# Kernel tuning notes

Hardware: AMD Instinct MI355X
Metric: run time of the kernel (lower is better)

## Reference

```python
import jax, jax.numpy as jnp
import numpy as np

B, H, W, C, NH, WS, SS = 16, 112, 112, 384, 12, 7, 3
HD = C // NH          # head dim = 32
N = WS * WS           # tokens per window = 49
MLP_H = 4 * C         # 1536
NW = (H // WS) * (W // WS)  # windows per image = 256


def _rel_pos_index():
    coords = np.stack(np.meshgrid(np.arange(WS), np.arange(WS), indexing='ij')).reshape(2, -1)
    rel = (coords[:, :, None] - coords[:, None, :]).transpose(1, 2, 0)  # (N, N, 2)
    rel[..., 0] += WS - 1
    rel[..., 1] += WS - 1
    rel[..., 0] *= 2 * WS - 1
    return rel.sum(-1)  # (N, N) in [0, (2WS-1)^2)


def _attn_mask():
    img = np.zeros((H, W))
    cnt = 0
    slices = (slice(0, -WS), slice(-WS, -SS), slice(-SS, None))
    for hs in slices:
        for ws_ in slices:
            img[hs, ws_] = cnt
            cnt += 1
    mw = img.reshape(H // WS, WS, W // WS, WS).transpose(0, 2, 1, 3).reshape(-1, N)
    am = mw[:, None, :] - mw[:, :, None]
    return np.where(am != 0, -100.0, 0.0).astype(np.float32)  # (NW, N, N)


REL_IDX = jnp.asarray(_rel_pos_index().reshape(-1))  # (N*N,) int
MASK = jnp.asarray(_attn_mask())                      # (NW, N, N)


def _ln(x, g, b, eps=1e-5):
    m = jnp.mean(x, -1, keepdims=True)
    v = jnp.mean((x - m) ** 2, -1, keepdims=True)
    return (x - m) / jnp.sqrt(v + eps) * g + b


def setup_inputs() -> dict:
    key = jax.random.key(0)
    ks = jax.random.split(key, 16)
    s = 0.02
    return {
        'x': jax.random.normal(ks[0], (B, H * W, C), jnp.float32),
        'norm1_g': jnp.ones((C,), jnp.float32),
        'norm1_b': jnp.zeros((C,), jnp.float32),
        'qkv_w': jax.random.normal(ks[1], (C, 3 * C), jnp.float32) * s,
        'qkv_b': jnp.zeros((3 * C,), jnp.float32),
        'proj_w': jax.random.normal(ks[2], (C, C), jnp.float32) * s,
        'proj_b': jnp.zeros((C,), jnp.float32),
        'rpb_table': jax.random.normal(ks[3], ((2 * WS - 1) ** 2, NH), jnp.float32) * s,
        'norm2_g': jnp.ones((C,), jnp.float32),
        'norm2_b': jnp.zeros((C,), jnp.float32),
        'fc1_w': jax.random.normal(ks[4], (C, MLP_H), jnp.float32) * s,
        'fc1_b': jnp.zeros((MLP_H,), jnp.float32),
        'fc2_w': jax.random.normal(ks[5], (MLP_H, C), jnp.float32) * s,
        'fc2_b': jnp.zeros((C,), jnp.float32),
    }


def reference(x, norm1_g, norm1_b, qkv_w, qkv_b, proj_w, proj_b, rpb_table,
              norm2_g, norm2_b, fc1_w, fc1_b, fc2_w, fc2_b):
    shortcut = x
    h = _ln(x, norm1_g, norm1_b).reshape(B, H, W, C)
    # cyclic shift
    h = jnp.roll(h, (-SS, -SS), axis=(1, 2))
    # window partition -> (B*NW, N, C)
    wins = h.reshape(B, H // WS, WS, W // WS, WS, C).transpose(0, 1, 3, 2, 4, 5).reshape(-1, N, C)
    qkv = (wins @ qkv_w + qkv_b).reshape(-1, N, 3, NH, HD).transpose(2, 0, 3, 1, 4)
    q, k, v = qkv[0] * HD ** -0.5, qkv[1], qkv[2]  # (B*NW, NH, N, HD)
    attn = jnp.einsum('bhnd,bhmd->bhnm', q, k)
    bias = rpb_table[REL_IDX].reshape(N, N, NH).transpose(2, 0, 1)  # (NH, N, N)
    attn = attn + bias[None]
    attn = (attn.reshape(B, NW, NH, N, N) + MASK[None, :, None]).reshape(-1, NH, N, N)
    attn = jax.nn.softmax(attn, axis=-1)
    out = jnp.einsum('bhnm,bhmd->bhnd', attn, v).transpose(0, 2, 1, 3).reshape(-1, N, C)
    out = out @ proj_w + proj_b
    # window reverse
    out = out.reshape(B, H // WS, W // WS, WS, WS, C).transpose(0, 1, 3, 2, 4, 5).reshape(B, H, W, C)
    out = jnp.roll(out, (SS, SS), axis=(1, 2)).reshape(B, H * W, C)
    x = shortcut + out
    h2 = _ln(x, norm2_g, norm2_b)
    h2 = jax.nn.gelu(h2 @ fc1_w + fc1_b, approximate=False) @ fc2_w + fc2_b
    return x + h2
```

## Files before the change

### kernel.cpp

```cpp
#include <hip/hip_runtime.h>
#include <hip/hip_bf16.h>

typedef short bf16x8 __attribute__((ext_vector_type(8)));
typedef float f32x4 __attribute__((ext_vector_type(4)));
typedef float f32x16 __attribute__((ext_vector_type(16)));
typedef unsigned int u32x4 __attribute__((ext_vector_type(4)));
typedef unsigned int u32x2 __attribute__((ext_vector_type(2)));

typedef __attribute__((address_space(1))) void gvoid;
typedef __attribute__((address_space(3))) void lvoid;

__device__ __forceinline__ short f2b(float f) {
  __hip_bfloat16 h = __float2bfloat16(f);
  return __builtin_bit_cast(short, h);
}

__device__ __forceinline__ f32x4 mfma16(bf16x8 a, bf16x8 b, f32x4 c) {
  return __builtin_amdgcn_mfma_f32_16x16x32_bf16(a, b, c, 0, 0, 0);
}

__device__ __forceinline__ f32x16 mfma32(bf16x8 a, bf16x8 b, f32x16 c) {
  return __builtin_amdgcn_mfma_f32_32x32x16_bf16(a, b, c, 0, 0, 0);
}

__device__ __forceinline__ unsigned cvtpk(float lo, float hi) {
  unsigned r;
  asm("v_cvt_pk_bf16_f32 %0, %1, %2" : "=v"(r) : "v"(lo), "v"(hi));
  return r;
}

__device__ __forceinline__ void gload16(const void* g, void* l) {
  __builtin_amdgcn_global_load_lds((const gvoid*)g, (lvoid*)l, 16, 0, 0);
}

__global__ __launch_bounds__(256) void convT_k(const float* __restrict__ src,
                                               short* __restrict__ dst, int K,
                                               int N, int scale_cols,
                                               float scale) {
  int idx = blockIdx.x * 256 + threadIdx.x;
  if (idx >= N * K) return;
  int n = idx / K, k = idx % K;
  float v = src[(size_t)k * N + n];
  if (n < scale_cols) v *= scale;
  dst[idx] = f2b(v);
}

__global__ __launch_bounds__(256) void scale_bias_k(const float* __restrict__ src,
                                                    float* __restrict__ dst,
                                                    int n, int scale_cols,
                                                    float scale) {
  int i = blockIdx.x * 256 + threadIdx.x;
  if (i >= n) return;
  dst[i] = src[i] * (i < scale_cols ? scale : 1.f);
}

__global__ __launch_bounds__(256) void biasmask_k(const float* __restrict__ rpb,
                                                  float* __restrict__ tbl) {
  int idx = blockIdx.x * 256 + threadIdx.x;
  int key = idx & 63, q = (idx >> 6) & 63;
  int hc = idx >> 12;
  int h = hc % 12, cls = hc / 12;
  float v;
  if (q >= 49 || key >= 49) {
    v = -1e4f;
  } else {
    int i1 = q / 7, j1 = q % 7, i2 = key / 7, j2 = key % 7;
    v = rpb[(size_t)((i1 - i2 + 6) * 13 + (j1 - j2 + 6)) * 12 + h];
    int clsh = cls >> 1, clsw = cls & 1;
    int rq = (clsh ? 1 + (i1 >= 4) : 0) * 3 + (clsw ? 1 + (j1 >= 4) : 0);
    int rk = (clsh ? 1 + (i2 >= 4) : 0) * 3 + (clsw ? 1 + (j2 >= 4) : 0);
    if (rq != rk) v -= 100.f;
  }
  tbl[idx] = v;
}

template <bool GATHER>
__device__ __forceinline__ void ln_body(const float* __restrict__ x,
                                        const float* __restrict__ gw,
                                        const float* __restrict__ bw,
                                        short* __restrict__ out) {
  const int lane = threadIdx.x & 63;
  const int t = (blockIdx.x << 2) + (threadIdx.x >> 6);
  size_t srow;
  if (GATHER) {
    int bb = t / 12544, rm2 = t % 12544;
    int wi = rm2 / 49, nn = rm2 % 49;
    int wh = wi >> 4, ww = wi & 15;
    int ii = nn / 7, jj = nn % 7;
    int rr = wh * 7 + ii + 3; if (rr >= 112) rr -= 112;
    int cc = ww * 7 + jj + 3; if (cc >= 112) cc -= 112;
    srow = ((size_t)bb * 12544 + rr * 112 + cc) * 384;
  } else {
    srow = (size_t)t * 384;
  }
  const float2* src = (const float2*)(x + srow);
  const float2* g2 = (const float2*)gw;
  const float2* b2 = (const float2*)bw;
  float2 u[3];
  float s = 0.f, ss = 0.f;
#pragma unroll
  for (int k = 0; k < 3; ++k) {
    u[k] = src[lane + (k << 6)];
    s += u[k].x + u[k].y;
    ss += u[k].x * u[k].x + u[k].y * u[k].y;
  }
#pragma unroll
  for (int m = 1; m < 64; m <<= 1) {
    s += __shfl_xor(s, m, 64);
    ss += __shfl_xor(ss, m, 64);
  }
  const float mean = s * (1.f / 384.f);
  const float var = ss * (1.f / 384.f) - mean * mean;
  const float rstd = rsqrtf(var + 1e-5f);
  unsigned* o = (unsigned*)(out + (size_t)t * 384);
#pragma unroll
  for (int k = 0; k < 3; ++k) {
    int c = lane + (k << 6);
    float2 gv = g2[c], bv = b2[c];
    unsigned lo = (unsigned short)f2b((u[k].x - mean) * rstd * gv.x + bv.x);
    unsigned hi = (unsigned short)f2b((u[k].y - mean) * rstd * gv.y + bv.y);
    o[c] = lo | (hi << 16);
  }
}

__global__ __launch_bounds__(256) void ln1_k(const float* __restrict__ x,
                                             const float* __restrict__ gw,
                                             const float* __restrict__ bw,
                                             short* __restrict__ out) {
  ln_body<true>(x, gw, bw, out);
}
__global__ __launch_bounds__(256) void ln2_k(const float* __restrict__ x,
                                             const float* __restrict__ gw,
                                             const float* __restrict__ bw,
                                             short* __restrict__ out) {
  ln_body<false>(x, gw, bw, out);
}

template <int EPI>
__device__ __forceinline__ void gemm_body(
    const short* __restrict__ A, int lda, const short* __restrict__ BT,
    int ldb, const float* __restrict__ bias, int K, short* __restrict__ outh,
    int ldo, float* __restrict__ outf, const float* __restrict__ resid) {
  __shared__ __align__(16) short A0s[8192], B0s[8192];
  __shared__ __align__(16) short A1s[8192], B1s[8192];
  const int tid = threadIdx.x;
  const int gx = gridDim.x;
  int lin = blockIdx.y * gx + blockIdx.x;
  const int cpx = (gx * gridDim.y) >> 3;
  lin = (lin & 7) * cpx + (lin >> 3);
  const int m0 = (lin / gx) << 7, n0 = (lin % gx) << 7;
  const int lane = tid & 63;
  const int wave = tid >> 6;
  const int wr = (wave >> 2) << 6;
  const int wc = (wave & 3) << 5;
  const int g = lane >> 4, q = lane & 15;
  const int q7 = q & 7;
  const int rd0 = ((g) ^ q7) << 3;
  const int rd1 = ((4 + g) ^ q7) << 3;
  const int cswz = ((tid & 7) ^ ((tid >> 3) & 7)) << 3;
  const int ldst = tid << 3;

  f32x4 acc[4][2];
#pragma unroll
  for (int i = 0; i < 4; ++i)
#pragma unroll
    for (int j = 0; j < 2; ++j) acc[i][j] = (f32x4){0.f, 0.f, 0.f, 0.f};

  const short* Abase = A + (size_t)(m0 + (tid >> 3)) * lda + cswz;
  const short* Bbase = BT + (size_t)(n0 + (tid >> 3)) * ldb + cswz;

#define STAGE(kt, DA, DB)                                        \
  do {                                                           \
    gload16(Abase + (kt), &DA[ldst]);                            \
    gload16(Abase + (size_t)64 * lda + (kt), &DA[4096 + ldst]);  \
    gload16(Bbase + (kt), &DB[ldst]);                            \
    gload16(Bbase + (size_t)64 * ldb + (kt), &DB[4096 + ldst]);  \
  } while (0)

#define COMPUTE(SA, SB)                                                       \
  do {                                                                        \
    _Pragma("unroll") for (int kk = 0; kk < 2; ++kk) {                        \
      const int rdo = kk ? rd1 : rd0;                                         \
      bf16x8 af[4], bfv[2];                                                   \
      _Pragma("unroll") for (int mi = 0; mi < 4; ++mi)                        \
          af[mi] = *(const bf16x8*)&SA[(wr + mi * 16 + q) * 64 + rdo];        \
      _Pragma("unroll") for (int ni = 0; ni < 2; ++ni)                        \
          bfv[ni] = *(const bf16x8*)&SB[(wc + ni * 16 + q) * 64 + rdo];       \
      _Pragma("unroll") for (int mi = 0; mi < 4; ++mi)                        \
          _Pragma("unroll") for (int ni = 0; ni < 2; ++ni)                    \
              acc[mi][ni] = mfma16(bfv[ni], af[mi], acc[mi][ni]);             \
    }                                                                         \
  } while (0)

  const int nt = K >> 6;
  STAGE(0, A0s, B0s);
  __syncthreads();
  for (int t = 0; t < nt; t += 2) {
    STAGE((t + 1) << 6, A1s, B1s);
    COMPUTE(A0s, B0s);
    __syncthreads();
    if (t + 2 < nt) STAGE((t + 2) << 6, A0s, B0s);
    COMPUTE(A1s, B1s);
    __syncthreads();
  }
#undef STAGE
#undef COMPUTE

  f32x4 bq[2];
#pragma unroll
  for (int ni = 0; ni < 2; ++ni)
    bq[ni] = bias ? *(const f32x4*)&bias[n0 + wc + ni * 16 + g * 4]
                  : (f32x4){0.f, 0.f, 0.f, 0.f};

#pragma unroll
  for (int mi = 0; mi < 4; ++mi) {
    const int grow = m0 + wr + mi * 16 + q;
    size_t orow;
    if constexpr (EPI == 2) {
      int bb = grow / 12544, rm2 = grow % 12544;
      int wi = rm2 / 49, nn = rm2 % 49;
      int wh = wi >> 4, ww = wi & 15;
      int ii = nn / 7, jj = nn % 7;
      int rr = wh * 7 + ii + 3; if (rr >= 112) rr -= 112;
      int cc = ww * 7 + jj + 3; if (cc >= 112) cc -= 112;
      orow = ((size_t)bb * 12544 + rr * 112 + cc) * 384;
    } else {
      orow = (size_t)grow * (size_t)ldo;
    }
#pragma unroll
    for (int ni = 0; ni < 2; ++ni) {
      const int gcol = n0 + wc + ni * 16 + g * 4;
      float v[4];
#pragma unroll
      for (int j = 0; j < 4; ++j) v[j] = acc[mi][ni][j] + bq[ni][j];
      if constexpr (EPI == 0) {
        u32x2 u = {cvtpk(v[0], v[1]), cvtpk(v[2], v[3])};
        *(u32x2*)&outh[orow + gcol] = u;
      } else if constexpr (EPI == 1) {
#pragma unroll
        for (int j = 0; j < 4; ++j)
          v[j] = 0.5f * v[j] * (1.f + erff(v[j] * 0.70710678118f));
        u32x2 u = {cvtpk(v[0], v[1]), cvtpk(v[2], v[3])};
        *(u32x2*)&outh[orow + gcol] = u;
      } else if constexpr (EPI == 2) {
        f32x4 r = *(const f32x4*)&resid[orow + gcol];
#pragma unroll
        for (int j = 0; j < 4; ++j) r[j] += v[j];
        *(f32x4*)&outf[orow + gcol] = r;
      } else {
        f32x4 o = *(f32x4*)&outf[orow + gcol];
#pragma unroll
        for (int j = 0; j < 4; ++j) o[j] += v[j];
        *(f32x4*)&outf[orow + gcol] = o;
      }
    }
  }
}

#define GEMM_WRAP(NAME, EPI)                                                   \
  __global__ __launch_bounds__(512) void NAME(                                 \
      const short* __restrict__ A, int lda, const short* __restrict__ BT,      \
      int ldb, const float* __restrict__ bias, int K,                          \
      short* __restrict__ outh, int ldo, float* __restrict__ outf,             \
      const float* __restrict__ resid) {                                       \
    gemm_body<EPI>(A, lda, BT, ldb, bias, K, outh, ldo, outf, resid);          \
  }
GEMM_WRAP(gemm_qkv_k, 0)
GEMM_WRAP(gemm_fc1_k, 1)
GEMM_WRAP(gemm_proj_k, 2)
GEMM_WRAP(gemm_fc2_k, 3)

__global__ __launch_bounds__(256) void attn_k(const short* __restrict__ qkv,
                                              const float* __restrict__ tbl,
                                              short* __restrict__ out) {
  const int lane = threadIdx.x & 63;
  const int task = blockIdx.x * 4 + (threadIdx.x >> 6);
  const int win = task / 12;
  const int h = task - win * 12;
  const int wh = (win >> 4) & 15, ww = win & 15;
  const int cls = ((wh == 15) ? 2 : 0) + ((ww == 15) ? 1 : 0);
  const int l31 = lane & 31, h5 = lane >> 5;
  const size_t tokbase = (size_t)win * 49;
  const short* base = qkv + tokbase * 1152 + h * 32;
  const bf16x8 zero8 = {0, 0, 0, 0, 0, 0, 0, 0};

  bf16x8 kf[2][2];
#pragma unroll
  for (int mi = 0; mi < 2; ++mi) {
    int row = l31 + 32 * mi;
#pragma unroll
    for (int s = 0; s < 2; ++s)
      kf[mi][s] = (row < 49)
                      ? *(const bf16x8*)(base + (size_t)row * 1152 + 384 +
                                         16 * s + 8 * h5)
                      : zero8;
  }
  bf16x8 vf[4];
#pragma unroll
  for (int kt = 0; kt < 4; ++kt) {
#pragma unroll
    for (int e = 0; e < 8; ++e) {
      int key = 16 * kt + 8 * h5 + e;
      vf[kt][e] = (key < 49) ? base[(size_t)key * 1152 + 768 + l31] : (short)0;
    }
  }

  const float* tb = tbl + ((size_t)(cls * 12 + h) << 12);

#pragma unroll
  for (int ni = 0; ni < 2; ++ni) {
    bf16x8 qf[2];
    int qrow = l31 + 32 * ni;
#pragma unroll
    for (int s = 0; s < 2; ++s)
      qf[s] = (qrow < 49)
                  ? *(const bf16x8*)(base + (size_t)qrow * 1152 + 16 * s +
                                     8 * h5)
                  : zero8;
    f32x16 st[2];
#pragma unroll
    for (int mi = 0; mi < 2; ++mi) {
      st[mi] = mfma32(kf[mi][0], qf[0], (f32x16)(0.f));
      st[mi] = mfma32(kf[mi][1], qf[1], st[mi]);
    }
#pragma unroll
    for (int mi = 0; mi < 2; ++mi) {
      const float* bp = tb + (size_t)(32 * ni + l31) * 64 + 32 * mi + 4 * h5;
#pragma unroll
      for (int j = 0; j < 4; ++j) {
        f32x4 b4 = *(const f32x4*)(bp + 8 * j);
#pragma unroll
        for (int e = 0; e < 4; ++e) st[mi][4 * j + e] += b4[e];
      }
    }
    float mx = st[0][0];
#pragma unroll
    for (int r = 1; r < 16; ++r) mx = fmaxf(mx, st[0][r]);
#pragma unroll
    for (int r = 0; r < 16; ++r) mx = fmaxf(mx, st[1][r]);
    mx = fmaxf(mx, __shfl_xor(mx, 32, 64));
    float sm = 0.f;
#pragma unroll
    for (int mi = 0; mi < 2; ++mi)
#pragma unroll
      for (int r = 0; r < 16; ++r) {
        float e = __expf(st[mi][r] - mx);
        st[mi][r] = e;
        sm += e;
      }
    sm += __shfl_xor(sm, 32, 64);
    const float rinv = 1.f / sm;
#pragma unroll
    for (int mi = 0; mi < 2; ++mi)
#pragma unroll
      for (int r = 0; r < 16; ++r) st[mi][r] *= rinv;

    f32x16 acc = (f32x16)(0.f);
#pragma unroll
    for (int kt = 0; kt < 4; ++kt) {
      const int mi = kt >> 1, b8 = (kt & 1) * 8;
      unsigned q0l = cvtpk(st[mi][b8 + 0], st[mi][b8 + 1]);
      unsigned q0h = cvtpk(st[mi][b8 + 2], st[mi][b8 + 3]);
      unsigned q1l = cvtpk(st[mi][b8 + 4], st[mi][b8 + 5]);
      unsigned q1h = cvtpk(st[mi][b8 + 6], st[mi][b8 + 7]);
      unsigned sl = h5 ? q0l : q1l, sh = h5 ? q0h : q1h;
      unsigned kl = h5 ? q1l : q0l, kh = h5 ? q1h : q0h;
      unsigned rl = (unsigned)__shfl_xor((int)sl, 32, 64);
      unsigned rh = (unsigned)__shfl_xor((int)sh, 32, 64);
      u32x4 fr;
      fr[0] = h5 ? rl : kl;
      fr[1] = h5 ? rh : kh;
      fr[2] = h5 ? kl : rl;
      fr[3] = h5 ? kh : rh;
      acc = mfma32(__builtin_bit_cast(bf16x8, fr), vf[kt], acc);
    }
#pragma unroll
    for (int r = 0; r < 16; ++r) {
      int query = 32 * ni + (r & 3) + 8 * (r >> 2) + 4 * h5;
      if (ni == 0 || query < 49)
        out[(tokbase + query) * 384 + h * 32 + l31] = f2b(acc[r]);
    }
  }
}

extern "C" void kernel_launch(void* const* d_in, const int* in_sizes, int n_in,
                              void* d_out, int out_size, void* d_ws,
                              size_t ws_size, hipStream_t stream) {
  const float* x = (const float*)d_in[0];
  const float* n1g = (const float*)d_in[1];
  const float* n1b = (const float*)d_in[2];
  const float* qkvw = (const float*)d_in[3];
  const float* qkvb = (const float*)d_in[4];
  const float* projw = (const float*)d_in[5];
  const float* projb = (const float*)d_in[6];
  const float* rpb = (const float*)d_in[7];
  const float* n2g = (const float*)d_in[8];
  const float* n2b = (const float*)d_in[9];
  const float* fc1w = (const float*)d_in[10];
  const float* fc1b = (const float*)d_in[11];
  const float* fc2w = (const float*)d_in[12];
  const float* fc2b = (const float*)d_in[13];
  float* out = (float*)d_out;

  char* ws = (char*)d_ws;
  short* w_qkvT = (short*)(ws + 0);
  short* w_projT = (short*)(ws + 884736);
  short* w_fc1T = (short*)(ws + 1179648);
  short* w_fc2T = (short*)(ws + 2359296);
  float* w_qb = (float*)(ws + 3538944);
  float* tbl = (float*)(ws + 3543552);
  const size_t o_qkv = 4329984;
  short* qkvbuf = (short*)(ws + o_qkv);
  const size_t o_hwin = o_qkv + 462422016ull;
  short* hwin = (short*)(ws + o_hwin);
  short* fc1c = hwin;
  short* h2 = qkvbuf;

  const float qscale = 0.17677669529663687f;

  convT_k<<<(442368 + 255) / 256, 256, 0, stream>>>(qkvw, w_qkvT, 384, 1152, 384, qscale);
  convT_k<<<(147456 + 255) / 256, 256, 0, stream>>>(projw, w_projT, 384, 384, 0, 1.f);
  convT_k<<<(589824 + 255) / 256, 256, 0, stream>>>(fc1w, w_fc1T, 384, 1536, 0, 1.f);
  convT_k<<<(589824 + 255) / 256, 256, 0, stream>>>(fc2w, w_fc2T, 1536, 384, 0, 1.f);
  scale_bias_k<<<5, 256, 0, stream>>>(qkvb, w_qb, 1152, 384, qscale);
  biasmask_k<<<768, 256, 0, stream>>>(rpb, tbl);

  ln1_k<<<50176, 256, 0, stream>>>(x, n1g, n1b, hwin);
  gemm_qkv_k<<<dim3(9, 1568), 512, 0, stream>>>(hwin, 384, w_qkvT, 384, w_qb,
                                                384, qkvbuf, 1152, nullptr,
                                                nullptr);
  attn_k<<<12288, 256, 0, stream>>>(qkvbuf, tbl, hwin);
  gemm_proj_k<<<dim3(3, 1568), 512, 0, stream>>>(hwin, 384, w_projT, 384,
                                                 projb, 384, nullptr, 384, out,
                                                 x);
  ln2_k<<<50176, 256, 0, stream>>>(out, n2g, n2b, h2);
  for (int s = 0; s < 4; ++s) {
    const size_t ro = (size_t)s * 50176;
    gemm_fc1_k<<<dim3(12, 392), 512, 0, stream>>>(
        h2 + ro * 384, 384, w_fc1T, 384, fc1b, 384, fc1c, 1536, nullptr,
        nullptr);
    gemm_fc2_k<<<dim3(3, 392), 512, 0, stream>>>(
        fc1c, 1536, w_fc2T, 1536, fc2b, 1536, nullptr, 384, out + ro * 384,
        nullptr);
  }
}
```

Before: 1.812 ms.

## Use 256x128 tiles with BK=32 for QKV and proj GEMMs

New measurement: 1.812 ms. About the same (+0.0%).

```diff
diff --git a/kernel.cpp b/kernel.cpp
--- a/kernel.cpp
+++ b/kernel.cpp
@@ -31,6 +31,13 @@
 
 __device__ __forceinline__ void gload16(const void* g, void* l) {
   __builtin_amdgcn_global_load_lds((const gvoid*)g, (lvoid*)l, 16, 0, 0);
+}
+
+__device__ __forceinline__ int xcd_bijective(int lin, int nwg) {
+  const int xcd = lin & 7, idx = lin >> 3;
+  const int q0 = nwg >> 3, r0 = nwg & 7;
+  return (xcd < r0) ? xcd * (q0 + 1) + idx
+                    : r0 * (q0 + 1) + (xcd - r0) * q0 + idx;
 }
 
 __global__ __launch_bounds__(256) void convT_k(const float* __restrict__ src,
@@ -137,7 +144,50 @@
 }
 
 template <int EPI>
-__device__ __forceinline__ void gemm_body(
+__device__ __forceinline__ void epi_store(int grow, int gcol, int ldo,
+                                          f32x4 av, f32x4 bq,
+                                          short* __restrict__ outh,
+                                          float* __restrict__ outf,
+                                          const float* __restrict__ resid) {
+  size_t orow;
+  if constexpr (EPI == 2) {
+    int bb = grow / 12544, rm2 = grow % 12544;
+    int wi = rm2 / 49, nn = rm2 % 49;
+    int wh = wi >> 4, ww = wi & 15;
+    int ii = nn / 7, jj = nn % 7;
+    int rr = wh * 7 + ii + 3; if (rr >= 112) rr -= 112;
+    int cc = ww * 7 + jj + 3; if (cc >= 112) cc -= 112;
+    orow = ((size_t)bb * 12544 + rr * 112 + cc) * 384;
+  } else {
+    orow = (size_t)grow * (size_t)ldo;
+  }
+  float v[4];
+#pragma unroll
+  for (int j = 0; j < 4; ++j) v[j] = av[j] + bq[j];
+  if constexpr (EPI == 0) {
+    u32x2 u = {cvtpk(v[0], v[1]), cvtpk(v[2], v[3])};
+    *(u32x2*)&outh[orow + gcol] = u;
+  } else if constexpr (EPI == 1) {
+#pragma unroll
+    for (int j = 0; j < 4; ++j)
+      v[j] = 0.5f * v[j] * (1.f + erff(v[j] * 0.70710678118f));
+    u32x2 u = {cvtpk(v[0], v[1]), cvtpk(v[2], v[3])};
+    *(u32x2*)&outh[orow + gcol] = u;
+  } else if constexpr (EPI == 2) {
+    f32x4 r = *(const f32x4*)&resid[orow + gcol];
+#pragma unroll
+    for (int j = 0; j < 4; ++j) r[j] += v[j];
+    *(f32x4*)&outf[orow + gcol] = r;
+  } else {
+    f32x4 o = *(f32x4*)&outf[orow + gcol];
+#pragma unroll
+    for (int j = 0; j < 4; ++j) o[j] += v[j];
+    *(f32x4*)&outf[orow + gcol] = o;
+  }
+}
+
+template <int EPI>
+__device__ __forceinline__ void gemm_bodyA(
     const short* __restrict__ A, int lda, const short* __restrict__ BT,
     int ldb, const float* __restrict__ bias, int K, short* __restrict__ outh,
     int ldo, float* __restrict__ outf, const float* __restrict__ resid) {
@@ -145,9 +195,7 @@
   __shared__ __align__(16) short A1s[8192], B1s[8192];
   const int tid = threadIdx.x;
   const int gx = gridDim.x;
-  int lin = blockIdx.y * gx + blockIdx.x;
-  const int cpx = (gx * gridDim.y) >> 3;
-  lin = (lin & 7) * cpx + (lin >> 3);
+  int lin = xcd_bijective(blockIdx.y * gx + blockIdx.x, gx * gridDim.y);
   const int m0 = (lin / gx) << 7, n0 = (lin % gx) << 7;
   const int lane = tid & 63;
   const int wave = tid >> 6;
@@ -215,60 +263,103 @@
 #pragma unroll
   for (int mi = 0; mi < 4; ++mi) {
     const int grow = m0 + wr + mi * 16 + q;
-    size_t orow;
-    if constexpr (EPI == 2) {
-      int bb = grow / 12544, rm2 = grow % 12544;
-      int wi = rm2 / 49, nn = rm2 % 49;
-      int wh = wi >> 4, ww = wi & 15;
-      int ii = nn / 7, jj = nn % 7;
-      int rr = wh * 7 + ii + 3; if (rr >= 112) rr -= 112;
-      int cc = ww * 7 + jj + 3; if (cc >= 112) cc -= 112;
-      orow = ((size_t)bb * 12544 + rr * 112 + cc) * 384;
-    } else {
-      orow = (size_t)grow * (size_t)ldo;
-    }
-#pragma unroll
-    for (int ni = 0; ni < 2; ++ni) {
-      const int gcol = n0 + wc + ni * 16 + g * 4;
-      float v[4];
-#pragma unroll
-      for (int j = 0; j < 4; ++j) v[j] = acc[mi][ni][j] + bq[ni][j];
-      if constexpr (EPI == 0) {
-        u32x2 u = {cvtpk(v[0], v[1]), cvtpk(v[2], v[3])};
-        *(u32x2*)&outh[orow + gcol] = u;
-      } else if constexpr (EPI == 1) {
-#pragma unroll
-        for (int j = 0; j < 4; ++j)
-          v[j] = 0.5f * v[j] * (1.f + erff(v[j] * 0.70710678118f));
-        u32x2 u = {cvtpk(v[0], v[1]), cvtpk(v[2], v[3])};
-        *(u32x2*)&outh[orow + gcol] = u;
-      } else if constexpr (EPI == 2) {
-        f32x4 r = *(const f32x4*)&resid[orow + gcol];
-#pragma unroll
-        for (int j = 0; j < 4; ++j) r[j] += v[j];
-        *(f32x4*)&outf[orow + gcol] = r;
-      } else {
-        f32x4 o = *(f32x4*)&outf[orow + gcol];
-#pragma unroll
-        for (int j = 0; j < 4; ++j) o[j] += v[j];
-        *(f32x4*)&outf[orow + gcol] = o;
-      }
-    }
-  }
-}
-
-#define GEMM_WRAP(NAME, EPI)                                                   \
+#pragma unroll
+    for (int ni = 0; ni < 2; ++ni)
+      epi_store<EPI>(grow, n0 + wc + ni * 16 + g * 4, ldo, acc[mi][ni],
+                     bq[ni], outh, outf, resid);
+  }
+}
+
+template <int EPI>
+__device__ __forceinline__ void gemm_bodyB(
+    const short* __restrict__ A, int lda, const short* __restrict__ BT,
+    int ldb, const float* __restrict__ bias, int K, short* __restrict__ outh,
+    int ldo, float* __restrict__ outf, const float* __restrict__ resid) {
+  __shared__ __align__(16) short A0s[8192], B0s[4096];
+  __shared__ __align__(16) short A1s[8192], B1s[4096];
+  const int tid = threadIdx.x;
+  const int gx = gridDim.x;
+  int lin = xcd_bijective(blockIdx.y * gx + blockIdx.x, gx * gridDim.y);
+  const int m0 = (lin / gx) << 8, n0 = (lin % gx) << 7;
+  const int lane = tid & 63;
+  const int wave = tid >> 6;
+  const int wr = (wave >> 1) << 6;
+  const int wc = (wave & 1) << 6;
+  const int g = lane >> 4, q = lane & 15;
+  const int rdo = ((g ^ ((q >> 1) & 3)) << 3);
+  const int gc = ((tid & 3) ^ ((tid >> 3) & 3)) << 3;
+  const int ldst = tid << 3;
+
+  f32x4 acc[4][4];
+#pragma unroll
+  for (int i = 0; i < 4; ++i)
+#pragma unroll
+    for (int j = 0; j < 4; ++j) acc[i][j] = (f32x4){0.f, 0.f, 0.f, 0.f};
+
+  const short* Abase = A + (size_t)(m0 + (tid >> 2)) * lda + gc;
+  const short* Bbase = BT + (size_t)(n0 + (tid >> 2)) * ldb + gc;
+
+#define STAGE(kt, DA, DB)                                         \
+  do {                                                            \
+    gload16(Abase + (kt), &DA[ldst]);                             \
+    gload16(Abase + (size_t)128 * lda + (kt), &DA[4096 + ldst]);  \
+    gload16(Bbase + (kt), &DB[ldst]);                             \
+  } while (0)
+
+#define COMPUTE(SA, SB)                                                       \
+  do {                                                                        \
+    bf16x8 af[4], bfv[4];                                                     \
+    _Pragma("unroll") for (int mi = 0; mi < 4; ++mi)                          \
+        af[mi] = *(const bf16x8*)&SA[(wr + mi * 16 + q) * 32 + rdo];          \
+    _Pragma("unroll") for (int ni = 0; ni < 4; ++ni)                          \
+        bfv[ni] = *(const bf16x8*)&SB[(wc + ni * 16 + q) * 32 + rdo];         \
+    _Pragma("unroll") for (int mi = 0; mi < 4; ++mi)                          \
+        _Pragma("unroll") for (int ni = 0; ni < 4; ++ni)                      \
+            acc[mi][ni] = mfma16(bfv[ni], af[mi], acc[mi][ni]);               \
+  } while (0)
+
+  const int nt = K >> 5;
+  STAGE(0, A0s, B0s);
+  __syncthreads();
+  for (int t = 0; t < nt; t += 2) {
+    STAGE((t + 1) << 5, A1s, B1s);
+    COMPUTE(A0s, B0s);
+    __syncthreads();
+    if (t + 2 < nt) STAGE((t + 2) << 5, A0s, B0s);
+    COMPUTE(A1s, B1s);
+    __syncthreads();
+  }
+#undef STAGE
+#undef COMPUTE
+
+  f32x4 bq[4];
+#pragma unroll
+  for (int ni = 0; ni < 4; ++ni)
+    bq[ni] = bias ? *(const f32x4*)&bias[n0 + wc + ni * 16 + g * 4]
+                  : (f32x4){0.f, 0.f, 0.f, 0.f};
+
+#pragma unroll
+  for (int mi = 0; mi < 4; ++mi) {
+    const int grow = m0 + wr + mi * 16 + q;
+#pragma unroll
+    for (int ni = 0; ni < 4; ++ni)
+      epi_store<EPI>(grow, n0 + wc + ni * 16 + g * 4, ldo, acc[mi][ni],
+                     bq[ni], outh, outf, resid);
+  }
+}
+
+#define GEMM_WRAP(NAME, BODY, EPI)                                             \
   __global__ __launch_bounds__(512) void NAME(                                 \
       const short* __restrict__ A, int lda, const short* __restrict__ BT,      \
       int ldb, const float* __restrict__ bias, int K,                          \
       short* __restrict__ outh, int ldo, float* __restrict__ outf,             \
       const float* __restrict__ resid) {                                       \
-    gemm_body<EPI>(A, lda, BT, ldb, bias, K, outh, ldo, outf, resid);          \
-  }
-GEMM_WRAP(gemm_qkv_k, 0)
-GEMM_WRAP(gemm_fc1_k, 1)
-GEMM_WRAP(gemm_proj_k, 2)
-GEMM_WRAP(gemm_fc2_k, 3)
+    BODY<EPI>(A, lda, BT, ldb, bias, K, outh, ldo, outf, resid);               \
+  }
+GEMM_WRAP(gemm_qkv_k, gemm_bodyB, 0)
+GEMM_WRAP(gemm_proj_k, gemm_bodyB, 2)
+GEMM_WRAP(gemm_fc1_k, gemm_bodyA, 1)
+GEMM_WRAP(gemm_fc2_k, gemm_bodyA, 3)
 
 __global__ __launch_bounds__(256) void attn_k(const short* __restrict__ qkv,
                                               const float* __restrict__ tbl,
@@ -426,13 +517,13 @@
   biasmask_k<<<768, 256, 0, stream>>>(rpb, tbl);
 
   ln1_k<<<50176, 256, 0, stream>>>(x, n1g, n1b, hwin);
-  gemm_qkv_k<<<dim3(9, 1568), 512, 0, stream>>>(hwin, 384, w_qkvT, 384, w_qb,
-                                                384, qkvbuf, 1152, nullptr,
-                                                nullptr);
+  gemm_qkv_k<<<dim3(9, 784), 512, 0, stream>>>(hwin, 384, w_qkvT, 384, w_qb,
+                                               384, qkvbuf, 1152, nullptr,
+                                               nullptr);
   attn_k<<<12288, 256, 0, stream>>>(qkvbuf, tbl, hwin);
-  gemm_proj_k<<<dim3(3, 1568), 512, 0, stream>>>(hwin, 384, w_projT, 384,
-                                                 projb, 384, nullptr, 384, out,
-                                                 x);
+  gemm_proj_k<<<dim3(3, 784), 512, 0, stream>>>(hwin, 384, w_projT, 384,
+                                                projb, 384, nullptr, 384, out,
+                                                x);
   ln2_k<<<50176, 256, 0, stream>>>(out, n2g, n2b, h2);
   for (int s = 0; s < 4; ++s) {
     const size_t ro = (size_t)s * 50176;
```
